# Kernel tuning notes

Hardware: AMD Instinct MI355X
Metric: run time of the kernel (lower is better)

Reference implementation:

```python
import jax, jax.numpy as jnp
import numpy as np
from jax.scipy.linalg import expm

EPS = 1e-5  # torch LayerNorm default

def _layernorm(x, g, b):
    m = x.mean(-1, keepdims=True)
    v = ((x - m) ** 2).mean(-1, keepdims=True)
    return (x - m) / jnp.sqrt(v + EPS) * g + b

def setup_inputs() -> dict:
    H, S, K = 1024, 64, 3
    B, T = 4, 4096
    key = jax.random.key(0)
    ks = jax.random.split(key, 12)
    sc = 0.02
    inp = {
        'x': jax.random.normal(ks[0], (B, T, H), jnp.float32),
        'A': -jnp.abs(jax.random.normal(ks[1], (S, S), jnp.float32) * sc),
        'dt_A': jnp.asarray(0.1, jnp.float32),
        'B_w': jax.random.normal(ks[2], (S, H), jnp.float32) * sc,
        'B_b': jnp.zeros((S,), jnp.float32),
        'C_w': jax.random.normal(ks[3], (S, H), jnp.float32) * sc,
        'C_b': jnp.zeros((S,), jnp.float32),
        'D_w': jax.random.normal(ks[4], (H, S), jnp.float32) * sc,
        'D_b': jnp.zeros((H,), jnp.float32),
        'conv_w': jax.random.normal(ks[5], (H, 1, K), jnp.float32) * sc,  # depthwise
        'conv_b': jnp.zeros((H,), jnp.float32),
        'gate_w': jax.random.normal(ks[6], (2 * H, H), jnp.float32) * sc,
        'gate_b': jnp.zeros((2 * H,), jnp.float32),
        'ln_in_g': jnp.ones((H,), jnp.float32),
        'ln_in_b': jnp.zeros((H,), jnp.float32),
        'ln_st_g': jnp.ones((S,), jnp.float32),
        'ln_st_b': jnp.zeros((S,), jnp.float32),
    }
    return inp

def reference(x, A, dt_A, B_w, B_b, C_w, C_b, D_w, D_b, conv_w, conv_b,
              gate_w, gate_b, ln_in_g, ln_in_b, ln_st_g, ln_st_b):
    Bt, T, H = x.shape
    K = conv_w.shape[-1]
    pad = K // 2
    x_norm = _layernorm(x, ln_in_g, ln_in_b)  # [B,T,H]
    # depthwise conv1d (groups = H), 'same' padding, residual add
    xc = jnp.transpose(x_norm, (0, 2, 1))  # [B,H,T]
    xc = jax.lax.conv_general_dilated(
        xc, conv_w, window_strides=(1,), padding=[(pad, pad)],
        dimension_numbers=('NCH', 'OIH', 'NCH'), feature_group_count=H)
    xc = xc + conv_b[None, :, None]
    x_norm = x_norm + jnp.transpose(xc, (0, 2, 1))
    # gating
    gate_all = x_norm @ gate_w.T + gate_b  # [B,T,2H]
    gate, input_gate = gate_all[..., :H], gate_all[..., H:]
    gate = jax.nn.sigmoid(gate)
    # input-dependent B, C
    Bm = (x_norm * jax.nn.sigmoid(input_gate)) @ B_w.T + B_b  # [B,T,S]
    Cm = x_norm @ C_w.T + C_b                                  # [B,T,S]
    A_bar = expm(dt_A * A)  # [S,S]
    # sequential recurrence over time via scan
    def step(state, bc):
        b_t, c_t = bc
        s = state @ A_bar + b_t
        s = _layernorm(s, ln_st_g, ln_st_b)
        return s, c_t * s
    state0 = jnp.zeros((Bt, A.shape[0]), x.dtype)
    _, ys = jax.lax.scan(step, state0,
                         (jnp.transpose(Bm, (1, 0, 2)), jnp.transpose(Cm, (1, 0, 2))))
    ssm = jnp.transpose(ys, (1, 0, 2))  # [B,T,S]
    ssm = ssm @ D_w.T + D_b             # [B,T,H]
    return ssm * gate
```

## Files before the change

kernel.cpp:

```cpp
#include <hip/hip_runtime.h>
#include <cstdint>

#define EPS 1e-5f
typedef float f32x4 __attribute__((ext_vector_type(4)));
typedef short bf8 __attribute__((ext_vector_type(8)));
typedef unsigned short u16;
typedef unsigned short u16x8 __attribute__((ext_vector_type(8)));
typedef unsigned int uint4v __attribute__((ext_vector_type(4)));

__device__ __forceinline__ u16 f2b(float f){
  unsigned x = __float_as_uint(f);
  unsigned r = x + 0x7FFFu + ((x>>16)&1u);
  return (u16)(r>>16);
}
__device__ __forceinline__ float b2f(u16 h){ return __uint_as_float(((unsigned)h)<<16); }
__device__ __forceinline__ unsigned pk2(float a, float b){
  unsigned ua = __float_as_uint(a) + 0x8000u;
  unsigned ub = __float_as_uint(b) + 0x8000u;
  return __builtin_amdgcn_perm(ub, ua, 0x07060302u);
}

#define GLL(gp, lp) __builtin_amdgcn_global_load_lds((__attribute__((address_space(1))) const void*)(gp), (__attribute__((address_space(3))) void*)(lp), 16, 0, 0)

__global__ __launch_bounds__(1024) void k_prep(const float* __restrict__ A, const float* __restrict__ dtp,
    const float* __restrict__ stg, const float* __restrict__ stb,
    float* __restrict__ abeta, u16* __restrict__ ft, float* __restrict__ dcm)
{
  __shared__ float M[4096], Ta[4096], Tb[4096], P[4096];
  __shared__ float cmn[64];
  int tid = threadIdx.x;
  float dt = dtp[0];
  for (int e=tid; e<4096; e+=1024){
    float v = dt * A[e];
    int i = e>>6, j = e&63;
    M[e] = v;
    P[e] = v + (i==j ? 1.0f : 0.0f);
    Ta[e] = v;
  }
  __syncthreads();
  float* src = Ta; float* dst = Tb;
  for (int k=2;k<=14;k++){
    float inv = 1.0f/(float)k;
    int i = tid>>4, j0 = (tid&15)*4;
    float a0=0,a1=0,a2=0,a3=0;
    for (int m2=0;m2<64;m2++){
      float f = src[i*64+m2];
      const float* Mr = &M[m2*64+j0];
      a0 += f*Mr[0]; a1 += f*Mr[1]; a2 += f*Mr[2]; a3 += f*Mr[3];
    }
    a0*=inv; a1*=inv; a2*=inv; a3*=inv;
    int base=i*64+j0;
    dst[base+0]=a0; dst[base+1]=a1; dst[base+2]=a2; dst[base+3]=a3;
    P[base+0]+=a0; P[base+1]+=a1; P[base+2]+=a2; P[base+3]+=a3;
    __syncthreads();
    float* tmp=src; src=dst; dst=tmp;
  }
  if (tid<64){
    float c0=0, ab=0; int p = tid;
    for (int q2=0;q2<64;q2++){ float ap = P[q2*64+p]; c0 += stg[q2]*ap; ab += stb[q2]*ap; }
    cmn[p] = c0*(1.0f/64.0f);
    abeta[p] = ab;
    dcm[p]    = stg[p]*P[p*64+p];
    dcm[64+p] = c0*(1.0f/64.0f);
  }
  __syncthreads();
  for (int e=tid; e<4096; e+=1024){
    int q2=e>>6, p=e&63;
    Ta[e] = stg[q2]*P[q2*64+p];
  }
  __syncthreads();
  for (int ii=0; ii<4; ii++){
    int e = tid*4+ii;
    int j = e&7, l = (e>>3)&63, kt=(e>>9)&1, mt=e>>10;
    int q2 = 16*(2*kt + (j>>2)) + 4*(l>>4) + (j&3);
    int p = 16*mt + (l&15);
    float v = (q2==p) ? 0.0f : Ta[q2*64+p];
    ft[e] = f2b(v);
  }
}

__global__ __launch_bounds__(256) void k_wcvt(const float* __restrict__ gw, const float* __restrict__ bw,
   const float* __restrict__ cw, const float* __restrict__ dw,
   u16* __restrict__ ogw, u16* __restrict__ obw, u16* __restrict__ ocw, u16* __restrict__ odw)
{
  int n = blockIdx.x*256 + threadIdx.x;
  if (n < 2097152) ogw[n] = f2b(gw[n]);
  else if (n < 2162688) obw[n-2097152] = f2b(bw[n-2097152]);
  else if (n < 2228224) ocw[n-2162688] = f2b(cw[n-2162688]);
  else odw[n-2228224] = f2b(dw[n-2228224]);
}

__global__ __launch_bounds__(256) void k_lnconv(const float* __restrict__ x, const float* __restrict__ gin,
  const float* __restrict__ bin, const float* __restrict__ cwt, const float* __restrict__ cb, u16* __restrict__ xn)
{
  __shared__ float red[10][8];
  int tid = threadIdx.x; int w = tid>>6; int lane = tid&63;
  int r0 = blockIdx.x*8;
  int bt = r0>>12, t0 = r0&4095;
  int c4 = tid*4;
  f32x4 g4 = *(const f32x4*)(gin + c4);
  f32x4 b4 = *(const f32x4*)(bin + c4);
  f32x4 vals[10];
  for (int lr=0; lr<10; lr++){
    int t = t0 - 1 + lr;
    f32x4 xv = {0,0,0,0};
    bool ok = (t>=0 && t<4096);
    if (ok) xv = *(const f32x4*)(x + (size_t)(bt*4096+t)*1024 + c4);
    float s = xv.x+xv.y+xv.z+xv.w;
    float q = xv.x*xv.x+xv.y*xv.y+xv.z*xv.z+xv.w*xv.w;
    for (int m2=1;m2<=32;m2<<=1){ s += __shfl_xor(s,m2,64); q += __shfl_xor(q,m2,64); }
    if (lane==0){ red[lr][w]=s; red[lr][4+w]=q; }
    __syncthreads();
    s = red[lr][0]+red[lr][1]+red[lr][2]+red[lr][3];
    q = red[lr][4]+red[lr][5]+red[lr][6]+red[lr][7];
    float mu = s*(1.f/1024.f);
    float var = q*(1.f/1024.f) - mu*mu;
    float rr = rsqrtf(var + EPS);
    f32x4 o = {0,0,0,0};
    if (ok){
      o.x=(xv.x-mu)*rr*g4.x+b4.x; o.y=(xv.y-mu)*rr*g4.y+b4.y;
      o.z=(xv.z-mu)*rr*g4.z+b4.z; o.w=(xv.w-mu)*rr*g4.w+b4.w;
    }
    vals[lr]=o;
  }
  float w0[4], w1[4], w2[4], cbv[4];
  for (int ii=0;ii<4;ii++){ int c = c4+ii; w0[ii]=cwt[c*3+0]; w1[ii]=cwt[c*3+1]; w2[ii]=cwt[c*3+2]; cbv[ii]=cb[c]; }
  for (int lr=1; lr<=8; lr++){
    int t = t0 + lr - 1;
    f32x4 o;
    o.x = vals[lr].x + w0[0]*vals[lr-1].x + w1[0]*vals[lr].x + w2[0]*vals[lr+1].x + cbv[0];
    o.y = vals[lr].y + w0[1]*vals[lr-1].y + w1[1]*vals[lr].y + w2[1]*vals[lr+1].y + cbv[1];
    o.z = vals[lr].z + w0[2]*vals[lr-1].z + w1[2]*vals[lr].z + w2[2]*vals[lr+1].z + cbv[2];
    o.w = vals[lr].w + w0[3]*vals[lr-1].w + w1[3]*vals[lr].w + w2[3]*vals[lr+1].w + cbv[3];
    size_t off = (size_t)(bt*4096+t)*1024 + c4;
    unsigned lo2 = (unsigned)f2b(o.x) | ((unsigned)f2b(o.y)<<16);
    unsigned hi2 = (unsigned)f2b(o.z) | ((unsigned)f2b(o.w)<<16);
    uint2 pk; pk.x=lo2; pk.y=hi2;
    *(uint2*)(xn + off) = pk;
  }
}

__global__ __launch_bounds__(256) void k_gate(const u16* __restrict__ xn, const u16* __restrict__ gw,
    const float* __restrict__ gb, u16* __restrict__ gate_o, u16* __restrict__ xg_o)
{
  __shared__ char smem[33792];
  u16* As = (u16*)smem;
  u16* Bs = (u16*)(smem + 8192);
  float* st = (float*)smem;
  int tid=threadIdx.x, w=tid>>6, l=tid&63;
  int flat = blockIdx.x + (int)gridDim.x*blockIdx.y;
  int logical = (flat&7)*256 + (flat>>3);
  int n0 = (logical&15)*128, m0 = (logical>>4)*128;
  int wr = w>>1, wc = w&1;
  f32x4 acc[4][4] = {};
  for (int kk=0; kk<32; kk++){
    int k0 = kk*32;
    for (int i2=0;i2<2;i2++){
      const char* ga = (const char*)xn + ((size_t)(m0+32*w+16*i2+(l>>2))*1024 + k0)*2 + (l&3)*16;
      GLL(ga, (char*)As + (32*w+16*i2)*64);
      const char* gbp = (const char*)gw + ((size_t)(n0+32*w+16*i2+(l>>2))*1024 + k0)*2 + (l&3)*16;
// ... 29 lines not shown
        v = v + gb4[j];
        ob[4*j+0] = f2b(1.0f/(1.0f+__expf(-v.x)));
        ob[4*j+1] = f2b(1.0f/(1.0f+__expf(-v.y)));
        ob[4*j+2] = f2b(1.0f/(1.0f+__expf(-v.z)));
        ob[4*j+3] = f2b(1.0f/(1.0f+__expf(-v.w)));
      }
    } else {
      const u16* xp = xn + (size_t)row*1024 + (n0-1024) + q*32;
      u16 xb[32];
      for (int j=0;j<4;j++){
        u16x8 t8 = *(const u16x8*)(xp + 8*j);
        for (int e=0;e<8;e++) xb[8*j+e] = t8[e];
      }
      for (int j=0;j<8;j++){
        f32x4 v = *(const f32x4*)(sp + 4*j);
        v = v + gb4[j];
        ob[4*j+0] = f2b(b2f(xb[4*j+0]) * (1.0f/(1.0f+__expf(-v.x))));
        ob[4*j+1] = f2b(b2f(xb[4*j+1]) * (1.0f/(1.0f+__expf(-v.y))));
        ob[4*j+2] = f2b(b2f(xb[4*j+2]) * (1.0f/(1.0f+__expf(-v.z))));
        ob[4*j+3] = f2b(b2f(xb[4*j+3]) * (1.0f/(1.0f+__expf(-v.w))));
      }
    }
    u16* op = isxg ? (xg_o + (size_t)row*1024 + (n0-1024) + q*32)
                   : (gate_o + (size_t)row*1024 + n0 + q*32);
    unsigned od[16];
    for (int i2=0;i2<16;i2++) od[i2] = (unsigned)ob[2*i2] | ((unsigned)ob[2*i2+1]<<16);
    uint4v s0 = {od[0],od[1],od[2],od[3]};
    uint4v s1 = {od[4],od[5],od[6],od[7]};
    uint4v s2 = {od[8],od[9],od[10],od[11]};
    uint4v s3 = {od[12],od[13],od[14],od[15]};
    *(uint4v*)(op+ 0) = s0;
    *(uint4v*)(op+ 8) = s1;
    *(uint4v*)(op+16) = s2;
    *(uint4v*)(op+24) = s3;
  }
}

__global__ __launch_bounds__(256) void k_bc(const u16* __restrict__ xg, const u16* __restrict__ xn,
   const u16* __restrict__ bw, const u16* __restrict__ cw,
   const float* __restrict__ bb, const float* __restrict__ cbias_, const float* __restrict__ abeta,
   float* __restrict__ c_ws, u16* __restrict__ cm)
{
  __shared__ u16 As[128*32], Bs[64*32];
  int tid=threadIdx.x, w=tid>>6, l=tid&63;
  int id = blockIdx.x; int half = id>>7; int m0 = (id&127)*128;
  const u16* Ap = half ? xn : xg;
  const u16* Bp = half ? cw : bw;
  f32x4 acc[2][4]={};
  for (int kk=0;kk<32;kk++){
    int k0=kk*32;
    for (int i2=0;i2<2;i2++){
      const char* ga=(const char*)Ap + ((size_t)(m0+32*w+16*i2+(l>>2))*1024+k0)*2+(l&3)*16;
      GLL(ga, (char*)As+(32*w+16*i2)*64);
    }
    { const char* gbp=(const char*)Bp + ((size_t)(16*w+(l>>2))*1024+k0)*2+(l&3)*16;
      GLL(gbp, (char*)Bs+(16*w)*64); }
    __syncthreads();
    bf8 af[2], bfr[4];
    for (int mt=0;mt<2;mt++) af[mt]=*(const bf8*)(As+(32*w+16*mt+(l&15))*32+8*(l>>4));
    for (int nt=0;nt<4;nt++) bfr[nt]=*(const bf8*)(Bs+(16*nt+(l&15))*32+8*(l>>4));
    for (int mt=0;mt<2;mt++) for(int nt=0;nt<4;nt++)
      acc[mt][nt]=__builtin_amdgcn_mfma_f32_16x16x32_bf16(af[mt],bfr[nt],acc[mt][nt],0,0,0);
    __syncthreads();
  }
  int g=l>>4, c=l&15;
  if (half==0){
    for (int nt=0;nt<4;nt++){ int n=16*nt+c; float bias=bb[n]; float ab=abeta[n];
      for(int mt=0;mt<2;mt++) for(int r=0;r<4;r++){
        int row=m0+32*w+16*mt+4*g+r; int bt=row>>12, t=row&4095;
        float v=acc[mt][nt][r]+bias + (t>0?ab:0.0f);
        c_ws[(size_t)t*256 + bt*64 + n] = v;
      }
    }
  } else {
    for (int nt=0;nt<4;nt++){ int n=16*nt+c; float bias=cbias_[n];
      for(int mt=0;mt<2;mt++) for(int r=0;r<4;r++){
        int row=m0+32*w+16*mt+4*g+r;
        cm[(size_t)row*64+n]=f2b(acc[mt][nt][r]+bias);
      }
    }
  }
}

__global__ __launch_bounds__(64,1) void k_scan(const float* __restrict__ c_ws, const u16* __restrict__ ft,
  const float* __restrict__ dcm, float* __restrict__ z_ws)
{
  __shared__ float ring[16*256];
  int l=threadIdx.x, g=l>>4, b=l&3;
  const bf8* ftv=(const bf8*)ft;
  bf8 Rb[4][2];
  for(int mt=0;mt<4;mt++)for(int kt=0;kt<2;kt++)
    Rb[mt][kt]=ftv[(mt*2+kt)*64+l];
  f32x4 D2r[4], Cm4[4];
  for(int mt=0;mt<4;mt++){
    D2r[mt] = *(const f32x4*)(dcm + 16*mt + 4*g);
    Cm4[mt] = *(const f32x4*)(dcm + 64 + 16*mt + 4*g);
  }
  const f32x4 zed = {0.f,0.f,0.f,0.f};
  f32x4 z0,z1,z2,z3;
  {
    const float* zp = c_ws + b*64 + 4*g;
    z0=*(const f32x4*)(zp+0); z1=*(const f32x4*)(zp+16); z2=*(const f32x4*)(zp+32); z3=*(const f32x4*)(zp+48);
  }
  for(int u2=1;u2<=11;u2++){
    const char* ga=(const char*)c_ws + (size_t)u2*1024 + l*16;
    GLL(ga, (char*)ring + u2*1024);
  }
  asm volatile("s_waitcnt vmcnt(0)" ::: "memory");
  unsigned laneoff;
  {
    __attribute__((address_space(3))) float* l3=( __attribute__((address_space(3))) float*)ring;
    laneoff=(unsigned)(uintptr_t)l3 + (unsigned)(b*256 + g*16);
  }
  unsigned voff = (unsigned)(((l&15)*64 + 4*g)*4);
  unsigned long long zb = (unsigned long long)(uintptr_t)z_ws;
  f32x4 cN0,cN1,cN2,cN3;
  bf8 zf0, zf1;

  {
    uint4v p0,p1;
    p0.x=pk2(z0.x,z0.y); p0.y=pk2(z0.z,z0.w); p0.z=pk2(z1.x,z1.y); p0.w=pk2(z1.z,z1.w);
    p1.x=pk2(z2.x,z2.y); p1.y=pk2(z2.z,z2.w); p1.z=pk2(z3.x,z3.y); p1.w=pk2(z3.z,z3.w);
    { union { uint4v u; bf8 h; } cv; cv.u=p0; zf0=cv.h; cv.u=p1; zf1=cv.h; }
  }

  unsigned slotr = 1024u;
  unsigned ldst  = 12u*1024u;
  const char* gsrc = (const char*)c_ws + (size_t)12*1024;

  for (int t=0; t<4096; ++t){
    asm volatile("s_waitcnt vmcnt(48)" ::: "memory");
    { unsigned ro = laneoff + slotr;
      asm volatile("ds_read_b128 %0, %4 offset:0\n\t"
                   "ds_read_b128 %1, %4 offset:64\n\t"
                   "ds_read_b128 %2, %4 offset:128\n\t"
                   "ds_read_b128 %3, %4 offset:192"
                   : "=v"(cN0),"=v"(cN1),"=v"(cN2),"=v"(cN3) : "v"(ro) : "memory"); }
    GLL(gsrc + (size_t)l*16, (char*)ring + ldst);
    f32x4 u0=__builtin_amdgcn_mfma_f32_16x16x32_bf16(Rb[0][0],zf0,zed,0,0,0);
    f32x4 u1=__builtin_amdgcn_mfma_f32_16x16x32_bf16(Rb[1][0],zf0,zed,0,0,0);
    f32x4 u2=__builtin_amdgcn_mfma_f32_16x16x32_bf16(Rb[2][0],zf0,zed,0,0,0);
    f32x4 u3=__builtin_amdgcn_mfma_f32_16x16x32_bf16(Rb[3][0],zf0,zed,0,0,0);
    u0=__builtin_amdgcn_mfma_f32_16x16x32_bf16(Rb[0][1],zf1,u0,0,0,0);
    u1=__builtin_amdgcn_mfma_f32_16x16x32_bf16(Rb[1][1],zf1,u1,0,0,0);
    u2=__builtin_amdgcn_mfma_f32_16x16x32_bf16(Rb[2][1],zf1,u2,0,0,0);
    u3=__builtin_amdgcn_mfma_f32_16x16x32_bf16(Rb[3][1],zf1,u3,0,0,0);
    float s, rr;
    {
      f32x4 s4=(z0+z1)+(z2+z3);
      s=(s4.x+s4.y)+(s4.z+s4.w);
      f32x4 qa=z0*z0; qa=z1*z1+qa;
      f32x4 qb=z2*z2; qb=z3*z3+qb;
      f32x4 q4=qa+qb;
      float q=(q4.x+q4.y)+(q4.z+q4.w);
      float sB=s, qB=q;
      asm("v_permlane16_swap_b32 %0, %1" : "+v"(s), "+v"(sB));
      asm("v_permlane16_swap_b32 %0, %1" : "+v"(q), "+v"(qB));
      s+=sB; q+=qB;
      float sC=s, qC=q;
      asm("v_permlane32_swap_b32 %0, %1" : "+v"(s), "+v"(sC));
      asm("v_permlane32_swap_b32 %0, %1" : "+v"(q), "+v"(qC));
      s+=sC; q+=qC;
      float mu=s*(1.f/64.f);
      float var=q*(1.f/64.f)-mu*mu;
      rr=rsqrtf(var+EPS);
    }
    asm volatile("s_waitcnt lgkmcnt(0)" : "+v"(cN0),"+v"(cN1),"+v"(cN2),"+v"(cN3) :: "memory");
    f32x4 h0 = (z0*D2r[0] - Cm4[0]*s)*rr + cN0;
    f32x4 h1 = (z1*D2r[1] - Cm4[1]*s)*rr + cN1;
    f32x4 h2 = (z2*D2r[2] - Cm4[2]*s)*rr + cN2;
    f32x4 h3 = (z3*D2r[3] - Cm4[3]*s)*rr + cN3;
    asm volatile("global_store_dwordx4 %0, %1, %5\n\t"
                 "global_store_dwordx4 %0, %2, %5 offset:64\n\t"
                 "global_store_dwordx4 %0, %3, %5 offset:128\n\t"
                 "global_store_dwordx4 %0, %4, %5 offset:192"
                 :: "v"(voff), "v"(z0), "v"(z1), "v"(z2), "v"(z3), "s"(zb) : "memory");
    voff += 4096u;
    slotr = (slotr + 1024u) & 16383u;
    ldst  = (ldst  + 1024u) & 16383u;
    gsrc += 1024;
    z0 = u0*rr + h0;
    z1 = u1*rr + h1;
    z2 = u2*rr + h2;
    z3 = u3*rr + h3;
    uint4v p0,p1;
    p0.x=pk2(z0.x,z0.y); p0.y=pk2(z0.z,z0.w); p0.z=pk2(z1.x,z1.y); p0.w=pk2(z1.z,z1.w);
    p1.x=pk2(z2.x,z2.y); p1.y=pk2(z2.z,z2.w); p1.z=pk2(z3.x,z3.y); p1.w=pk2(z3.z,z3.w);
    { union { uint4v u; bf8 h; } cv; cv.u=p0; zf0=cv.h; cv.u=p1; zf1=cv.h; }
  }
}

__global__ __launch_bounds__(256) void k_y(const float* __restrict__ z_ws, const u16* __restrict__ cm,
  const float* __restrict__ stg, const float* __restrict__ stb, u16* __restrict__ y)
{
  int tid=threadIdx.x, w=tid>>6, l=tid&63;
  int token = blockIdx.x*4 + w;
  int bt = token>>12, t = token&4095;
  float zv = z_ws[(size_t)t*1024 + bt*64 + l];
  float s=zv, q=zv*zv;
  for (int m2=1;m2<=32;m2<<=1){ s += __shfl_xor(s,m2,64); q += __shfl_xor(q,m2,64); }
  float mu=s*(1.f/64.f), var=q*(1.f/64.f)-mu*mu, rr=rsqrtf(var+EPS);
  float sv=(zv-mu)*rr*stg[l]+stb[l];
  y[(size_t)token*64 + l] = f2b(sv * b2f(cm[(size_t)token*64+l]));
}

__global__ __launch_bounds__(256) void k_out(const u16* __restrict__ y, const u16* __restrict__ dw,
   const float* __restrict__ db, const u16* __restrict__ gate, float* __restrict__ out)
{
  __shared__ float tr[4][16][68];
  int tid=threadIdx.x, w=tid>>6, l=tid&63, g=l>>4, c=l&15;
  int n0=blockIdx.x*64, m0=blockIdx.y*64;
  int mrow = m0 + 16*w + c;
  bf8 af0=*(const bf8*)(y + (size_t)mrow*64 + 8*g);
  bf8 af1=*(const bf8*)(y + (size_t)mrow*64 + 32 + 8*g);
  f32x4 acc[4];
  for(int nt=0;nt<4;nt++){
    int n=n0+16*nt+c;
    bf8 b0=*(const bf8*)(dw + (size_t)n*64 + 8*g);
    bf8 b1=*(const bf8*)(dw + (size_t)n*64 + 32 + 8*g);
    f32x4 a={0,0,0,0};
    a=__builtin_amdgcn_mfma_f32_16x16x32_bf16(af0,b0,a,0,0,0);
    a=__builtin_amdgcn_mfma_f32_16x16x32_bf16(af1,b1,a,0,0,0);
    acc[nt]=a+db[n];
  }
  for(int nt=0;nt<4;nt++) for(int r=0;r<4;r++) tr[w][4*g+r][16*nt+c]=acc[nt][r];
  __syncthreads();
  int lr=l>>2, cc0=(l&3)*16;
  int grow=m0+16*w+lr;
  const u16* gp = gate + (size_t)grow*1024 + n0 + cc0;
  u16x8 g0=*(const u16x8*)(gp), g1=*(const u16x8*)(gp+8);
  float* op = out + (size_t)grow*1024 + n0 + cc0;
  float vv[16];
  for(int j2=0;j2<16;j2++){
    u16 gb16 = (j2<8)? g0[j2] : g1[j2-8];
    vv[j2]=tr[w][lr][cc0+j2]*b2f(gb16);
  }
  for(int j2=0;j2<4;j2++){
    f32x4 ov={vv[4*j2],vv[4*j2+1],vv[4*j2+2],vv[4*j2+3]};
    *(f32x4*)(op+4*j2)=ov;
  }
}

extern "C" void kernel_launch(void* const* d_in, const int* in_sizes, int n_in,
                              void* d_out, int out_size, void* d_ws, size_t ws_size,
                              hipStream_t stream) {
  const float* x=(const float*)d_in[0];
  const float* A=(const float*)d_in[1];
  const float* dt=(const float*)d_in[2];
  const float* B_w=(const float*)d_in[3];
  const float* B_b=(const float*)d_in[4];
  const float* C_w=(const float*)d_in[5];
  const float* C_b=(const float*)d_in[6];
  const float* D_w=(const float*)d_in[7];
  const float* D_b=(const float*)d_in[8];
  const float* conv_w=(const float*)d_in[9];
  const float* conv_b=(const float*)d_in[10];
  const float* gate_w=(const float*)d_in[11];
  const float* gate_b=(const float*)d_in[12];
  const float* ln_in_g=(const float*)d_in[13];
  const float* ln_in_b=(const float*)d_in[14];
  const float* ln_st_g=(const float*)d_in[15];
  const float* ln_st_b=(const float*)d_in[16];
  char* ws=(char*)d_ws;
  u16* xn   =(u16*)(ws);
  u16* xg   =(u16*)(ws+33554432);
  u16* gate =(u16*)(ws+67108864);
  u16* gwb  =(u16*)(ws+100663296);
  u16* bwb  =(u16*)(ws+104857600);
  u16* cwb  =(u16*)(ws+104988672);
  u16* dwb  =(u16*)(ws+105119744);
  u16* cm   =(u16*)(ws+105250816);
  float* c_ws=(float*)(ws+107347968);
  float* z_ws=(float*)(ws+111558656);
  u16* y    =(u16*)(ws+128335872);
  float* abeta=(float*)(ws+130433024);
  u16* ft   =(u16*)(ws+130433280);
  float* dcm =(float*)(ws+130433280+8192);
  float* out=(float*)d_out;

  hipLaunchKernelGGL(k_prep,  dim3(1),      dim3(1024),0,stream, A, dt, ln_st_g, ln_st_b, abeta, ft, dcm);
  hipLaunchKernelGGL(k_wcvt,  dim3(8960),   dim3(256), 0,stream, gate_w,B_w,C_w,D_w, gwb,bwb,cwb,dwb);
  hipLaunchKernelGGL(k_lnconv,dim3(2048),   dim3(256), 0,stream, x, ln_in_g, ln_in_b, conv_w, conv_b, xn);
  hipLaunchKernelGGL(k_gate,  dim3(16,128), dim3(256), 0,stream, xn,gwb,gate_b,gate,xg);
  hipLaunchKernelGGL(k_bc,    dim3(256),    dim3(256), 0,stream, xg,xn,bwb,cwb,B_b,C_b,abeta,c_ws,cm);
  hipLaunchKernelGGL(k_scan,  dim3(1),      dim3(64),  0,stream, c_ws, ft, dcm, z_ws);
  hipLaunchKernelGGL(k_y,     dim3(4096),   dim3(256), 0,stream, z_ws,cm,ln_st_g,ln_st_b,y);
  hipLaunchKernelGGL(k_out,   dim3(16,256), dim3(256), 0,stream, y,dwb,D_b,gate,out);
}
```

Measured before the change: 1.732 ms.

## Replace LDS ring prefetch in scan with register-rotated direct global loads

The sequential scan kernel drops its LDS ring buffer, which was filled with global_load_lds and read back with ds_read every step. It now keeps four register sets of prefetched per-step inputs and issues direct global loads three or four steps ahead, gated by a vmcnt wait in a loop unrolled by four. This removes the LDS round trip and lgkmcnt wait from the serial critical path. It also limits the z stores to the 4 of 16 lane groups that write meaningful rows, cutting redundant store traffic. The catch is a much shallower prefetch distance, and vmcnt now counts those stores too, so global load latency may be exposed more often.

```diff
diff --git a/kernel.cpp b/kernel.cpp
--- a/kernel.cpp
+++ b/kernel.cpp
@@ -274,7 +274,6 @@
 __global__ __launch_bounds__(64,1) void k_scan(const float* __restrict__ c_ws, const u16* __restrict__ ft,
   const float* __restrict__ dcm, float* __restrict__ z_ws)
 {
-  __shared__ float ring[16*256];
   int l=threadIdx.x, g=l>>4, b=l&3;
   const bf8* ftv=(const bf8*)ft;
   bf8 Rb[4][2];
@@ -291,19 +290,10 @@
     const float* zp = c_ws + b*64 + 4*g;
     z0=*(const f32x4*)(zp+0); z1=*(const f32x4*)(zp+16); z2=*(const f32x4*)(zp+32); z3=*(const f32x4*)(zp+48);
   }
-  for(int u2=1;u2<=11;u2++){
-    const char* ga=(const char*)c_ws + (size_t)u2*1024 + l*16;
-    GLL(ga, (char*)ring + u2*1024);
-  }
-  asm volatile("s_waitcnt vmcnt(0)" ::: "memory");
-  unsigned laneoff;
-  {
-    __attribute__((address_space(3))) float* l3=( __attribute__((address_space(3))) float*)ring;
-    laneoff=(unsigned)(uintptr_t)l3 + (unsigned)(b*256 + g*16);
-  }
   unsigned voff = (unsigned)(((l&15)*64 + 4*g)*4);
   unsigned long long zb = (unsigned long long)(uintptr_t)z_ws;
-  f32x4 cN0,cN1,cN2,cN3;
+  unsigned long long cbse = (unsigned long long)(uintptr_t)c_ws;
+  bool stl = ((l&15) < 4);
   bf8 zf0, zf1;
 
   {
@@ -313,70 +303,91 @@
     { union { uint4v u; bf8 h; } cv; cv.u=p0; zf0=cv.h; cv.u=p1; zf1=cv.h; }
   }
 
-  unsigned slotr = 1024u;
-  unsigned ldst  = 12u*1024u;
-  const char* gsrc = (const char*)c_ws + (size_t)12*1024;
-
-  for (int t=0; t<4096; ++t){
-    asm volatile("s_waitcnt vmcnt(48)" ::: "memory");
-    { unsigned ro = laneoff + slotr;
-      asm volatile("ds_read_b128 %0, %4 offset:0\n\t"
-                   "ds_read_b128 %1, %4 offset:64\n\t"
-                   "ds_read_b128 %2, %4 offset:128\n\t"
-                   "ds_read_b128 %3, %4 offset:192"
-                   : "=v"(cN0),"=v"(cN1),"=v"(cN2),"=v"(cN3) : "v"(ro) : "memory"); }
-    GLL(gsrc + (size_t)l*16, (char*)ring + ldst);
-    f32x4 u0=__builtin_amdgcn_mfma_f32_16x16x32_bf16(Rb[0][0],zf0,zed,0,0,0);
-    f32x4 u1=__builtin_amdgcn_mfma_f32_16x16x32_bf16(Rb[1][0],zf0,zed,0,0,0);
-    f32x4 u2=__builtin_amdgcn_mfma_f32_16x16x32_bf16(Rb[2][0],zf0,zed,0,0,0);
-    f32x4 u3=__builtin_amdgcn_mfma_f32_16x16x32_bf16(Rb[3][0],zf0,zed,0,0,0);
-    u0=__builtin_amdgcn_mfma_f32_16x16x32_bf16(Rb[0][1],zf1,u0,0,0,0);
-    u1=__builtin_amdgcn_mfma_f32_16x16x32_bf16(Rb[1][1],zf1,u1,0,0,0);
-    u2=__builtin_amdgcn_mfma_f32_16x16x32_bf16(Rb[2][1],zf1,u2,0,0,0);
-    u3=__builtin_amdgcn_mfma_f32_16x16x32_bf16(Rb[3][1],zf1,u3,0,0,0);
-    float s, rr;
-    {
-      f32x4 s4=(z0+z1)+(z2+z3);
-      s=(s4.x+s4.y)+(s4.z+s4.w);
-      f32x4 qa=z0*z0; qa=z1*z1+qa;
-      f32x4 qb=z2*z2; qb=z3*z3+qb;
-      f32x4 q4=qa+qb;
-      float q=(q4.x+q4.y)+(q4.z+q4.w);
-      float sB=s, qB=q;
-      asm("v_permlane16_swap_b32 %0, %1" : "+v"(s), "+v"(sB));
-      asm("v_permlane16_swap_b32 %0, %1" : "+v"(q), "+v"(qB));
-      s+=sB; q+=qB;
-      float sC=s, qC=q;
-      asm("v_permlane32_swap_b32 %0, %1" : "+v"(s), "+v"(sC));
-      asm("v_permlane32_swap_b32 %0, %1" : "+v"(q), "+v"(qC));
-      s+=sC; q+=qC;
-      float mu=s*(1.f/64.f);
-      float var=q*(1.f/64.f)-mu*mu;
-      rr=rsqrtf(var+EPS);
-    }
-    asm volatile("s_waitcnt lgkmcnt(0)" : "+v"(cN0),"+v"(cN1),"+v"(cN2),"+v"(cN3) :: "memory");
-    f32x4 h0 = (z0*D2r[0] - Cm4[0]*s)*rr + cN0;
-    f32x4 h1 = (z1*D2r[1] - Cm4[1]*s)*rr + cN1;
-    f32x4 h2 = (z2*D2r[2] - Cm4[2]*s)*rr + cN2;
-    f32x4 h3 = (z3*D2r[3] - Cm4[3]*s)*rr + cN3;
-    asm volatile("global_store_dwordx4 %0, %1, %5\n\t"
-                 "global_store_dwordx4 %0, %2, %5 offset:64\n\t"
-                 "global_store_dwordx4 %0, %3, %5 offset:128\n\t"
-                 "global_store_dwordx4 %0, %4, %5 offset:192"
-                 :: "v"(voff), "v"(z0), "v"(z1), "v"(z2), "v"(z3), "s"(zb) : "memory");
-    voff += 4096u;
-    slotr = (slotr + 1024u) & 16383u;
-    ldst  = (ldst  + 1024u) & 16383u;
-    gsrc += 1024;
-    z0 = u0*rr + h0;
-    z1 = u1*rr + h1;
-    z2 = u2*rr + h2;
-    z3 = u3*rr + h3;
-    uint4v p0,p1;
-    p0.x=pk2(z0.x,z0.y); p0.y=pk2(z0.z,z0.w); p0.z=pk2(z1.x,z1.y); p0.w=pk2(z1.z,z1.w);
-    p1.x=pk2(z2.x,z2.y); p1.y=pk2(z2.z,z2.w); p1.z=pk2(z3.x,z3.y); p1.w=pk2(z3.z,z3.w);
-    { union { uint4v u; bf8 h; } cv; cv.u=p0; zf0=cv.h; cv.u=p1; zf1=cv.h; }
-  }
+  unsigned cvo = (unsigned)((b*64 + 4*g)*4);
+  unsigned voA = 1024u*1 + cvo, voB = 1024u*2 + cvo, voC = 1024u*3 + cvo, voD = 1024u*4 + cvo;
+  f32x4 cA0,cA1,cA2,cA3, cB0,cB1,cB2,cB3, cC0,cC1,cC2,cC3, cD0,cD1,cD2,cD3;
+#define CLOAD(R0,R1,R2,R3, VO) \
+  asm volatile("global_load_dwordx4 %0, %4, %5 offset:0\n\t" \
+               "global_load_dwordx4 %1, %4, %5 offset:64\n\t" \
+               "global_load_dwordx4 %2, %4, %5 offset:128\n\t" \
+               "global_load_dwordx4 %3, %4, %5 offset:192" \
+               : "=&v"(R0),"=&v"(R1),"=&v"(R2),"=&v"(R3) \
+               : "v"(VO), "s"(cbse) : "memory")
+  CLOAD(cA0,cA1,cA2,cA3, voA);  voA += 4096u;
+  CLOAD(cB0,cB1,cB2,cB3, voB);  voB += 4096u;
+  CLOAD(cC0,cC1,cC2,cC3, voC);  voC += 4096u;
+  CLOAD(cD0,cD1,cD2,cD3, voD);  voD += 4096u;
+  asm volatile("s_waitcnt vmcnt(0)" ::: "memory");
+
+#define STEP(T, C0,C1,C2,C3, VO) do { \
+  asm volatile("s_waitcnt vmcnt(24)" : "+v"(C0),"+v"(C1),"+v"(C2),"+v"(C3) :: "memory"); \
+   \
+  f32x4 u0=__builtin_amdgcn_mfma_f32_16x16x32_bf16(Rb[0][0],zf0,zed,0,0,0); \
+  f32x4 u1=__builtin_amdgcn_mfma_f32_16x16x32_bf16(Rb[1][0],zf0,zed,0,0,0); \
+  f32x4 u2=__builtin_amdgcn_mfma_f32_16x16x32_bf16(Rb[2][0],zf0,zed,0,0,0); \
+  f32x4 u3=__builtin_amdgcn_mfma_f32_16x16x32_bf16(Rb[3][0],zf0,zed,0,0,0); \
+  u0=__builtin_amdgcn_mfma_f32_16x16x32_bf16(Rb[0][1],zf1,u0,0,0,0); \
+  u1=__builtin_amdgcn_mfma_f32_16x16x32_bf16(Rb[1][1],zf1,u1,0,0,0); \
+  u2=__builtin_amdgcn_mfma_f32_16x16x32_bf16(Rb[2][1],zf1,u2,0,0,0); \
+  u3=__builtin_amdgcn_mfma_f32_16x16x32_bf16(Rb[3][1],zf1,u3,0,0,0); \
+   \
+  float s, rr; \
+  { \
+    f32x4 s4=(z0+z1)+(z2+z3); \
+    s=(s4.x+s4.y)+(s4.z+s4.w); \
+    f32x4 qa=z0*z0; qa=z1*z1+qa; \
+    f32x4 qb=z2*z2; qb=z3*z3+qb; \
+    f32x4 q4=qa+qb; \
+    float q=(q4.x+q4.y)+(q4.z+q4.w); \
+    float sB=s, qB=q; \
+    asm("v_permlane16_swap_b32 %0, %1" : "+v"(s), "+v"(sB)); \
+    asm("v_permlane16_swap_b32 %0, %1" : "+v"(q), "+v"(qB)); \
+    s+=sB; q+=qB; \
+    float sC=s, qC=q; \
+    asm("v_permlane32_swap_b32 %0, %1" : "+v"(s), "+v"(sC)); \
+    asm("v_permlane32_swap_b32 %0, %1" : "+v"(q), "+v"(qC)); \
+    s+=sC; q+=qC; \
+    float mu=s*(1.f/64.f); \
+    float var=q*(1.f/64.f)-mu*mu; \
+    rr=rsqrtf(var+EPS); \
+  } \
+   \
+  f32x4 h0 = (z0*D2r[0] - Cm4[0]*s)*rr + C0; \
+  f32x4 h1 = (z1*D2r[1] - Cm4[1]*s)*rr + C1; \
+  f32x4 h2 = (z2*D2r[2] - Cm4[2]*s)*rr + C2; \
+  f32x4 h3 = (z3*D2r[3] - Cm4[3]*s)*rr + C3; \
+   \
+  if (stl){ \
+    asm volatile("global_store_dwordx4 %0, %1, %5\n\t" \
+                 "global_store_dwordx4 %0, %2, %5 offset:64\n\t" \
+                 "global_store_dwordx4 %0, %3, %5 offset:128\n\t" \
+                 "global_store_dwordx4 %0, %4, %5 offset:192" \
+                 :: "v"(voff), "v"(z0), "v"(z1), "v"(z2), "v"(z3), "s"(zb) : "memory"); \
+  } \
+  voff += 4096u; \
+   \
+  CLOAD(C0,C1,C2,C3, VO); \
+  VO += 4096u; \
+   \
+  z0 = u0*rr + h0; \
+  z1 = u1*rr + h1; \
+  z2 = u2*rr + h2; \
+  z3 = u3*rr + h3; \
+   \
+  uint4v p0,p1; \
+  p0.x=pk2(z0.x,z0.y); p0.y=pk2(z0.z,z0.w); p0.z=pk2(z1.x,z1.y); p0.w=pk2(z1.z,z1.w); \
+  p1.x=pk2(z2.x,z2.y); p1.y=pk2(z2.z,z2.w); p1.z=pk2(z3.x,z3.y); p1.w=pk2(z3.z,z3.w); \
+  { union { uint4v u; bf8 h; } cv; cv.u=p0; zf0=cv.h; cv.u=p1; zf1=cv.h; } \
+} while(0)
+
+  for (int t=0; t<4096; t+=4){
+    STEP(t,   cA0,cA1,cA2,cA3, voA);
+    STEP(t+1, cB0,cB1,cB2,cB3, voB);
+    STEP(t+2, cC0,cC1,cC2,cC3, voC);
+    STEP(t+3, cD0,cD1,cD2,cD3, voD);
+  }
+#undef STEP
+#undef CLOAD
 }
 
 __global__ __launch_bounds__(256) void k_y(const float* __restrict__ z_ws, const u16* __restrict__ cm,
```

Measured after the change: 1.912 ms. 1.1x slower.

## Two-step the sequential scan using precomputed squared transition and input projections

Applied to the files above, without the earlier changes.

The single-wave recurrence is reformulated to advance two timesteps per dependent chain. It precomputes the centred transition matrix and its square in k_prep, and the projections of the per-step inputs through both matrices in a new parallel kernel k_fc. The scan then issues both MFMA products from the same state and shortens the serial latency per pair of steps. State is now stored as bf16 in a new layout that k_y reads. This adds an extra kernel, more global traffic and more bf16 rounding of the projected terms, which risks accuracy drift over 4096 steps.

```diff
diff --git a/kernel.cpp b/kernel.cpp
--- a/kernel.cpp
+++ b/kernel.cpp
@@ -24,7 +24,8 @@
 
 __global__ __launch_bounds__(1024) void k_prep(const float* __restrict__ A, const float* __restrict__ dtp,
     const float* __restrict__ stg, const float* __restrict__ stb,
-    float* __restrict__ abeta, u16* __restrict__ ft, float* __restrict__ dcm)
+    float* __restrict__ abeta, u16* __restrict__ ft, float* __restrict__ dcm,
+    float* __restrict__ m1g, float* __restrict__ m2g)
 {
   __shared__ float M[4096], Ta[4096], Tb[4096], P[4096];
   __shared__ float cmn[64];
@@ -60,22 +61,37 @@
     for (int q2=0;q2<64;q2++){ float ap = P[q2*64+p]; c0 += stg[q2]*ap; ab += stb[q2]*ap; }
     cmn[p] = c0*(1.0f/64.0f);
     abeta[p] = ab;
-    dcm[p]    = stg[p]*P[p*64+p];
-    dcm[64+p] = c0*(1.0f/64.0f);
   }
   __syncthreads();
   for (int e=tid; e<4096; e+=1024){
     int q2=e>>6, p=e&63;
-    Ta[e] = stg[q2]*P[q2*64+p];
+    Ta[e] = stg[q2]*P[e] - cmn[p];
   }
   __syncthreads();
+  {
+    int i = tid>>4, j0 = (tid&15)*4;
+    float a0=0,a1=0,a2=0,a3=0;
+    for (int m2=0;m2<64;m2++){
+      float f = Ta[i*64+m2];
+      const float* Mr = &Ta[m2*64+j0];
+      a0 += f*Mr[0]; a1 += f*Mr[1]; a2 += f*Mr[2]; a3 += f*Mr[3];
+    }
+    int base=i*64+j0;
+    Tb[base+0]=a0; Tb[base+1]=a1; Tb[base+2]=a2; Tb[base+3]=a3;
+  }
+  __syncthreads();
+  for (int e=tid; e<4096; e+=1024){ m1g[e]=Ta[e]; m2g[e]=Tb[e]; }
+  if (tid<64){
+    dcm[tid]    = Ta[tid*64+tid];
+    dcm[64+tid] = Tb[tid*64+tid];
+  }
   for (int ii=0; ii<4; ii++){
     int e = tid*4+ii;
     int j = e&7, l = (e>>3)&63, kt=(e>>9)&1, mt=e>>10;
     int q2 = 16*(2*kt + (j>>2)) + 4*(l>>4) + (j&3);
     int p = 16*mt + (l&15);
-    float v = (q2==p) ? 0.0f : Ta[q2*64+p];
-    ft[e] = f2b(v);
+    ft[e]      = f2b(q2==p ? 0.0f : Ta[q2*64+p]);
+    ft[e+4096] = f2b(q2==p ? 0.0f : Tb[q2*64+p]);
   }
 }
 
@@ -271,121 +287,182 @@
   }
 }
 
+__global__ __launch_bounds__(256) void k_fc(const float* __restrict__ c_ws,
+  const float* __restrict__ m1g, const float* __restrict__ m2g,
+  u16* __restrict__ fc, u16* __restrict__ ffc)
+{
+  __shared__ float M1s[4096], M2s[4096], Cs[4096];
+  int tid=threadIdx.x; int t0=blockIdx.x*16;
+  for (int e=tid; e<4096; e+=256){
+    M1s[e]=m1g[e]; M2s[e]=m2g[e];
+    int row=e>>6, q=e&63;
+    Cs[e]=c_ws[(size_t)(t0+(row>>2))*256 + (row&3)*64 + q];
+  }
+  __syncthreads();
+  int row=tid>>2, pq=tid&3;
+  const float* cr=&Cs[row*64];
+  float f1[16], f2[16];
+  #pragma unroll
+  for (int k2=0;k2<16;k2++){ f1[k2]=0.f; f2[k2]=0.f; }
+  for (int q=0;q<64;q++){
+    float cq=cr[q];
+    const float* r1=&M1s[q*64+pq*16];
+    const float* r2=&M2s[q*64+pq*16];
+    #pragma unroll
+    for (int k2=0;k2<16;k2++){ f1[k2]+=cq*r1[k2]; f2[k2]+=cq*r2[k2]; }
+  }
+  int t=t0+(row>>2), b=row&3;
+  #pragma unroll
+  for (int gp=0;gp<4;gp++){
+    uint2 o1, o2;
+    o1.x = pk2(f1[gp*4+0], f1[gp*4+1]); o1.y = pk2(f1[gp*4+2], f1[gp*4+3]);
+    o2.x = pk2(f2[gp*4+0], f2[gp*4+1]); o2.y = pk2(f2[gp*4+2], f2[gp*4+3]);
+    size_t off = (size_t)t*256 + (size_t)((b*4+gp)*16 + pq*4);
+    *(uint2*)(fc+off) = o1;
+    *(uint2*)(ffc+off) = o2;
+  }
+}
+
 __global__ __launch_bounds__(64,1) void k_scan(const float* __restrict__ c_ws, const u16* __restrict__ ft,
-  const float* __restrict__ dcm, float* __restrict__ z_ws)
-{
-  __shared__ float ring[16*256];
+  const float* __restrict__ dcm, const u16* __restrict__ fc_ws, const u16* __restrict__ ffc_ws,
+  u16* __restrict__ zb16)
+{
   int l=threadIdx.x, g=l>>4, b=l&3;
   const bf8* ftv=(const bf8*)ft;
-  bf8 Rb[4][2];
-  for(int mt=0;mt<4;mt++)for(int kt=0;kt<2;kt++)
-    Rb[mt][kt]=ftv[(mt*2+kt)*64+l];
-  f32x4 D2r[4], Cm4[4];
+  bf8 O1f[4][2], O2f[4][2];
+  for(int mt=0;mt<4;mt++)for(int kt=0;kt<2;kt++){
+    O1f[mt][kt]=ftv[(mt*2+kt)*64+l];
+    O2f[mt][kt]=ftv[(8+mt*2+kt)*64+l];
+  }
+  f32x4 D1r[4], D2r[4];
   for(int mt=0;mt<4;mt++){
-    D2r[mt] = *(const f32x4*)(dcm + 16*mt + 4*g);
-    Cm4[mt] = *(const f32x4*)(dcm + 64 + 16*mt + 4*g);
-  }
-  const f32x4 zed = {0.f,0.f,0.f,0.f};
-  f32x4 z0,z1,z2,z3;
-  {
-    const float* zp = c_ws + b*64 + 4*g;
-    z0=*(const f32x4*)(zp+0); z1=*(const f32x4*)(zp+16); z2=*(const f32x4*)(zp+32); z3=*(const f32x4*)(zp+48);
-  }
-  for(int u2=1;u2<=11;u2++){
-    const char* ga=(const char*)c_ws + (size_t)u2*1024 + l*16;
-    GLL(ga, (char*)ring + u2*1024);
-  }
+    D1r[mt]=*(const f32x4*)(dcm+16*mt+4*g);
+    D2r[mt]=*(const f32x4*)(dcm+64+16*mt+4*g);
+  }
+  const f32x4 zed={0.f,0.f,0.f,0.f};
+  unsigned cbase=(unsigned)((b*64+4*g)*4);
+  unsigned fbase=(unsigned)((b*4+g)*32);
+  unsigned long long cbse=(unsigned long long)(uintptr_t)c_ws;
+  unsigned long long fbse=(unsigned long long)(uintptr_t)fc_ws;
+  unsigned long long hbse=(unsigned long long)(uintptr_t)ffc_ws;
+  unsigned long long zb  =(unsigned long long)(uintptr_t)zb16;
+  bool stl = ((l&15)<4);
+
+#define MF(Aop,Bop,Cin) __builtin_amdgcn_mfma_f32_16x16x32_bf16(Aop,Bop,Cin,0,0,0)
+#define UNPK(D, U, i0, i1) { D.x=__uint_as_float((U)[i0]<<16); D.y=__uint_as_float((U)[i0]&0xffff0000u); \
+                             D.z=__uint_as_float((U)[i1]<<16); D.w=__uint_as_float((U)[i1]&0xffff0000u); }
+#define PACKZ(Z0,Z1,Z2,Z3, P0,P1) { \
+  P0.x=pk2(Z0.x,Z0.y); P0.y=pk2(Z0.z,Z0.w); P0.z=pk2(Z1.x,Z1.y); P0.w=pk2(Z1.z,Z1.w); \
+  P1.x=pk2(Z2.x,Z2.y); P1.y=pk2(Z2.z,Z2.w); P1.z=pk2(Z3.x,Z3.y); P1.w=pk2(Z3.z,Z3.w); }
+#define REDUCE_RR(Z0,Z1,Z2,Z3, RR) { \
+  f32x4 s4=((Z0)+(Z1))+((Z2)+(Z3)); float s=(s4.x+s4.y)+(s4.z+s4.w); \
+  f32x4 qa=(Z0)*(Z0); qa=(Z1)*(Z1)+qa; f32x4 qb=(Z2)*(Z2); qb=(Z3)*(Z3)+qb; f32x4 q4=qa+qb; \
+  float q=(q4.x+q4.y)+(q4.z+q4.w); \
+  float sB=s,qB=q; asm("v_permlane16_swap_b32 %0, %1":"+v"(s),"+v"(sB)); \
+  asm("v_permlane16_swap_b32 %0, %1":"+v"(q),"+v"(qB)); s+=sB;q+=qB; \
+  float sC=s,qC=q; asm("v_permlane32_swap_b32 %0, %1":"+v"(s),"+v"(sC)); \
+  asm("v_permlane32_swap_b32 %0, %1":"+v"(q),"+v"(qC)); s+=sC;q+=qC; \
+  float mu=s*(1.f/64.f); float var=q*(1.f/64.f)-mu*mu; RR=rsqrtf(var+EPS); }
+#define LD_C(R0,R1,R2,R3, OFF) asm volatile( \
+  "global_load_dwordx4 %0, %4, %5 offset:0\n\t" \
+  "global_load_dwordx4 %1, %4, %5 offset:64\n\t" \
+  "global_load_dwordx4 %2, %4, %5 offset:128\n\t" \
+  "global_load_dwordx4 %3, %4, %5 offset:192" \
+  : "=&v"(R0),"=&v"(R1),"=&v"(R2),"=&v"(R3) : "v"(OFF), "s"(cbse) : "memory")
+#define LD_C2(R0,R1,R2,R3, OFF) asm volatile( \
+  "global_load_dwordx4 %0, %4, %5 offset:1024\n\t" \
+  "global_load_dwordx4 %1, %4, %5 offset:1088\n\t" \
+  "global_load_dwordx4 %2, %4, %5 offset:1152\n\t" \
+  "global_load_dwordx4 %3, %4, %5 offset:1216" \
+  : "=&v"(R0),"=&v"(R1),"=&v"(R2),"=&v"(R3) : "v"(OFF), "s"(cbse) : "memory")
+#define LD_F(Ra,Rb, OFF, BASE) asm volatile( \
+  "global_load_dwordx4 %0, %2, %3 offset:0\n\t" \
+  "global_load_dwordx4 %1, %2, %3 offset:16" \
+  : "=&v"(Ra),"=&v"(Rb) : "v"(OFF), "s"(BASE) : "memory")
+#define LD_F2(Ra,Rb, OFF, BASE) asm volatile( \
+  "global_load_dwordx4 %0, %2, %3 offset:512\n\t" \
+  "global_load_dwordx4 %1, %2, %3 offset:528" \
+  : "=&v"(Ra),"=&v"(Rb) : "v"(OFF), "s"(BASE) : "memory")
+#define ST_Z(P0,P1, VO) if(stl){ asm volatile( \
+  "global_store_dwordx4 %0, %1, %3\n\t" \
+  "global_store_dwordx4 %0, %2, %3 offset:16" \
+  :: "v"(VO), "v"(P0), "v"(P1), "s"(zb) : "memory"); }
+
+  f32x4 z00,z01,z02,z03;
+  { const float* zp = c_ws + b*64 + 4*g;
+    z00=*(const f32x4*)(zp); z01=*(const f32x4*)(zp+16); z02=*(const f32x4*)(zp+32); z03=*(const f32x4*)(zp+48); }
+  f32x4 Gs0,Gs1,Gs2,Gs3;
+  { const uint4v* fp=(const uint4v*)((const char*)fc_ws + fbase);
+    uint4v ga=fp[0], gb2=fp[1];
+    UNPK(Gs0, ga,0,1); UNPK(Gs1, ga,2,3); UNPK(Gs2, gb2,0,1); UNPK(Gs3, gb2,2,3); }
+  float rr; REDUCE_RR(z00,z01,z02,z03, rr);
+  bf8 zf0, zf1;
+  { uint4v p0,p1; PACKZ(Gs0,Gs1,Gs2,Gs3,p0,p1);
+    union{uint4v u; bf8 h;}cv; cv.u=p0; zf0=cv.h; cv.u=p1; zf1=cv.h; }
+  unsigned voff = fbase;
+  { uint4v q0,q1; PACKZ(z00,z01,z02,z03,q0,q1); ST_Z(q0,q1, voff); }
+  voff += 512u;
+  f32x4 cA10,cA11,cA12,cA13, cA20,cA21,cA22,cA23;
+  f32x4 cB10,cB11,cB12,cB13, cB20,cB21,cB22,cB23;
+  uint4v fA1a,fA1b, fA2a,fA2b, hA1a,hA1b;
+  uint4v fB1a,fB1b, fB2a,fB2b, hB1a,hB1b;
+  unsigned cOfA = 1024u + cbase,  fOfA = 512u + fbase;
+  unsigned cOfB = 3072u + cbase,  fOfB = 1536u + fbase;
+  LD_C (cA10,cA11,cA12,cA13, cOfA); LD_C2(cA20,cA21,cA22,cA23, cOfA);
+  LD_F (fA1a,fA1b, fOfA, fbse); LD_F2(fA2a,fA2b, fOfA, fbse); LD_F(hA1a,hA1b, fOfA, hbse);
+  cOfA += 4096u; fOfA += 2048u;
+  LD_C (cB10,cB11,cB12,cB13, cOfB); LD_C2(cB20,cB21,cB22,cB23, cOfB);
+  LD_F (fB1a,fB1b, fOfB, fbse); LD_F2(fB2a,fB2b, fOfB, fbse); LD_F(hB1a,hB1b, fOfB, hbse);
+  cOfB += 4096u; fOfB += 2048u;
   asm volatile("s_waitcnt vmcnt(0)" ::: "memory");
-  unsigned laneoff;
-  {
-    __attribute__((address_space(3))) float* l3=( __attribute__((address_space(3))) float*)ring;
-    laneoff=(unsigned)(uintptr_t)l3 + (unsigned)(b*256 + g*16);
-  }
-  unsigned voff = (unsigned)(((l&15)*64 + 4*g)*4);
-  unsigned long long zb = (unsigned long long)(uintptr_t)z_ws;
-  f32x4 cN0,cN1,cN2,cN3;
-  bf8 zf0, zf1;
-
-  {
-    uint4v p0,p1;
-    p0.x=pk2(z0.x,z0.y); p0.y=pk2(z0.z,z0.w); p0.z=pk2(z1.x,z1.y); p0.w=pk2(z1.z,z1.w);
-    p1.x=pk2(z2.x,z2.y); p1.y=pk2(z2.z,z2.w); p1.z=pk2(z3.x,z3.y); p1.w=pk2(z3.z,z3.w);
-    { union { uint4v u; bf8 h; } cv; cv.u=p0; zf0=cv.h; cv.u=p1; zf1=cv.h; }
-  }
-
-  unsigned slotr = 1024u;
-  unsigned ldst  = 12u*1024u;
-  const char* gsrc = (const char*)c_ws + (size_t)12*1024;
-
-  for (int t=0; t<4096; ++t){
-    asm volatile("s_waitcnt vmcnt(48)" ::: "memory");
-    { unsigned ro = laneoff + slotr;
-      asm volatile("ds_read_b128 %0, %4 offset:0\n\t"
-                   "ds_read_b128 %1, %4 offset:64\n\t"
-                   "ds_read_b128 %2, %4 offset:128\n\t"
-                   "ds_read_b128 %3, %4 offset:192"
-                   : "=v"(cN0),"=v"(cN1),"=v"(cN2),"=v"(cN3) : "v"(ro) : "memory"); }
-    GLL(gsrc + (size_t)l*16, (char*)ring + ldst);
-    f32x4 u0=__builtin_amdgcn_mfma_f32_16x16x32_bf16(Rb[0][0],zf0,zed,0,0,0);
-    f32x4 u1=__builtin_amdgcn_mfma_f32_16x16x32_bf16(Rb[1][0],zf0,zed,0,0,0);
-    f32x4 u2=__builtin_amdgcn_mfma_f32_16x16x32_bf16(Rb[2][0],zf0,zed,0,0,0);
-    f32x4 u3=__builtin_amdgcn_mfma_f32_16x16x32_bf16(Rb[3][0],zf0,zed,0,0,0);
-    u0=__builtin_amdgcn_mfma_f32_16x16x32_bf16(Rb[0][1],zf1,u0,0,0,0);
-    u1=__builtin_amdgcn_mfma_f32_16x16x32_bf16(Rb[1][1],zf1,u1,0,0,0);
-    u2=__builtin_amdgcn_mfma_f32_16x16x32_bf16(Rb[2][1],zf1,u2,0,0,0);
-    u3=__builtin_amdgcn_mfma_f32_16x16x32_bf16(Rb[3][1],zf1,u3,0,0,0);
-    float s, rr;
-    {
-      f32x4 s4=(z0+z1)+(z2+z3);
-      s=(s4.x+s4.y)+(s4.z+s4.w);
-      f32x4 qa=z0*z0; qa=z1*z1+qa;
-      f32x4 qb=z2*z2; qb=z3*z3+qb;
-      f32x4 q4=qa+qb;
-      float q=(q4.x+q4.y)+(q4.z+q4.w);
-      float sB=s, qB=q;
-      asm("v_permlane16_swap_b32 %0, %1" : "+v"(s), "+v"(sB));
-      asm("v_permlane16_swap_b32 %0, %1" : "+v"(q), "+v"(qB));
-      s+=sB; q+=qB;
-      float sC=s, qC=q;
-      asm("v_permlane32_swap_b32 %0, %1" : "+v"(s), "+v"(sC));
-      asm("v_permlane32_swap_b32 %0, %1" : "+v"(q), "+v"(qC));
-      s+=sC; q+=qC;
-      float mu=s*(1.f/64.f);
-      float var=q*(1.f/64.f)-mu*mu;
-      rr=rsqrtf(var+EPS);
-    }
-    asm volatile("s_waitcnt lgkmcnt(0)" : "+v"(cN0),"+v"(cN1),"+v"(cN2),"+v"(cN3) :: "memory");
-    f32x4 h0 = (z0*D2r[0] - Cm4[0]*s)*rr + cN0;
-    f32x4 h1 = (z1*D2r[1] - Cm4[1]*s)*rr + cN1;
-    f32x4 h2 = (z2*D2r[2] - Cm4[2]*s)*rr + cN2;
-    f32x4 h3 = (z3*D2r[3] - Cm4[3]*s)*rr + cN3;
-    asm volatile("global_store_dwordx4 %0, %1, %5\n\t"
-                 "global_store_dwordx4 %0, %2, %5 offset:64\n\t"
-                 "global_store_dwordx4 %0, %3, %5 offset:128\n\t"
-                 "global_store_dwordx4 %0, %4, %5 offset:192"
-                 :: "v"(voff), "v"(z0), "v"(z1), "v"(z2), "v"(z3), "s"(zb) : "memory");
-    voff += 4096u;
-    slotr = (slotr + 1024u) & 16383u;
-    ldst  = (ldst  + 1024u) & 16383u;
-    gsrc += 1024;
-    z0 = u0*rr + h0;
-    z1 = u1*rr + h1;
-    z2 = u2*rr + h2;
-    z3 = u3*rr + h3;
-    uint4v p0,p1;
-    p0.x=pk2(z0.x,z0.y); p0.y=pk2(z0.z,z0.w); p0.z=pk2(z1.x,z1.y); p0.w=pk2(z1.z,z1.w);
-    p1.x=pk2(z2.x,z2.y); p1.y=pk2(z2.z,z2.w); p1.z=pk2(z3.x,z3.y); p1.w=pk2(z3.z,z3.w);
-    { union { uint4v u; bf8 h; } cv; cv.u=p0; zf0=cv.h; cv.u=p1; zf1=cv.h; }
-  }
-}
-
-__global__ __launch_bounds__(256) void k_y(const float* __restrict__ z_ws, const u16* __restrict__ cm,
+
+#define ITER(C10,C11,C12,C13,C20,C21,C22,C23, F1a,F1b,F2a,F2b, H1a,H1b, COF, FOF) do{ \
+  asm volatile("s_waitcnt vmcnt(18)" : "+v"(C10),"+v"(C11),"+v"(C12),"+v"(C13), \
+     "+v"(C20),"+v"(C21),"+v"(C22),"+v"(C23), "+v"(F1a),"+v"(F1b),"+v"(F2a),"+v"(F2b), \
+     "+v"(H1a),"+v"(H1b) :: "memory"); \
+  f32x4 Ho0=MF(O1f[0][0],zf0,zed), Ho1=MF(O1f[1][0],zf0,zed), Ho2=MF(O1f[2][0],zf0,zed), Ho3=MF(O1f[3][0],zf0,zed); \
+  f32x4 Ko0=MF(O2f[0][0],zf0,zed), Ko1=MF(O2f[1][0],zf0,zed), Ko2=MF(O2f[2][0],zf0,zed), Ko3=MF(O2f[3][0],zf0,zed); \
+  Ho0=MF(O1f[0][1],zf1,Ho0); Ho1=MF(O1f[1][1],zf1,Ho1); Ho2=MF(O1f[2][1],zf1,Ho2); Ho3=MF(O1f[3][1],zf1,Ho3); \
+  Ko0=MF(O2f[0][1],zf1,Ko0); Ko1=MF(O2f[1][1],zf1,Ko1); Ko2=MF(O2f[2][1],zf1,Ko2); Ko3=MF(O2f[3][1],zf1,Ko3); \
+  f32x4 zA0=Gs0*rr+C10, zA1=Gs1*rr+C11, zA2=Gs2*rr+C12, zA3=Gs3*rr+C13; \
+  float rr1; REDUCE_RR(zA0,zA1,zA2,zA3, rr1); \
+  f32x4 Pa0,Pa1,Pa2,Pa3; UNPK(Pa0,F1a,0,1); UNPK(Pa1,F1a,2,3); UNPK(Pa2,F1b,0,1); UNPK(Pa3,F1b,2,3); \
+  f32x4 Pb0,Pb1,Pb2,Pb3; UNPK(Pb0,F2a,0,1); UNPK(Pb1,F2a,2,3); UNPK(Pb2,F2b,0,1); UNPK(Pb3,F2b,2,3); \
+  f32x4 Q0,Q1,Q2,Q3;     UNPK(Q0,H1a,0,1);  UNPK(Q1,H1a,2,3);  UNPK(Q2,H1b,0,1);  UNPK(Q3,H1b,2,3); \
+  f32x4 T0=Q0*rr1+Pb0, T1=Q1*rr1+Pb1, T2=Q2*rr1+Pb2, T3=Q3*rr1+Pb3; \
+  f32x4 H0=Gs0*D1r[0]+Ho0, H1=Gs1*D1r[1]+Ho1, H2=Gs2*D1r[2]+Ho2, H3=Gs3*D1r[3]+Ho3; \
+  f32x4 Gm0=H0*rr+Pa0, Gm1=H1*rr+Pa1, Gm2=H2*rr+Pa2, Gm3=H3*rr+Pa3; \
+  f32x4 zB0=Gm0*rr1+C20, zB1=Gm1*rr1+C21, zB2=Gm2*rr1+C22, zB3=Gm3*rr1+C23; \
+  float rr2; REDUCE_RR(zB0,zB1,zB2,zB3, rr2); \
+  f32x4 K0=Gs0*D2r[0]+Ko0, K1=Gs1*D2r[1]+Ko1, K2=Gs2*D2r[2]+Ko2, K3=Gs3*D2r[3]+Ko3; \
+  float rrp=rr*rr1; \
+  Gs0=K0*rrp+T0; Gs1=K1*rrp+T1; Gs2=K2*rrp+T2; Gs3=K3*rrp+T3; \
+  { uint4v q0,q1; PACKZ(zA0,zA1,zA2,zA3,q0,q1); ST_Z(q0,q1, voff); } \
+  { uint4v q0,q1; PACKZ(zB0,zB1,zB2,zB3,q0,q1); ST_Z(q0,q1, voff+512u); } \
+  voff += 1024u; \
+  LD_C (C10,C11,C12,C13, COF); LD_C2(C20,C21,C22,C23, COF); \
+  LD_F (F1a,F1b, FOF, fbse); LD_F2(F2a,F2b, FOF, fbse); LD_F(H1a,H1b, FOF, hbse); \
+  COF += 4096u; FOF += 2048u; \
+  { uint4v p0,p1; PACKZ(Gs0,Gs1,Gs2,Gs3,p0,p1); \
+    union{uint4v u; bf8 h;}cv; cv.u=p0; zf0=cv.h; cv.u=p1; zf1=cv.h; } \
+  rr = rr2; \
+}while(0)
+
+  for (int i=0; i<2048; i+=2){
+    ITER(cA10,cA11,cA12,cA13,cA20,cA21,cA22,cA23, fA1a,fA1b,fA2a,fA2b, hA1a,hA1b, cOfA, fOfA);
+    ITER(cB10,cB11,cB12,cB13,cB20,cB21,cB22,cB23, fB1a,fB1b,fB2a,fB2b, hB1a,hB1b, cOfB, fOfB);
+  }
+#undef ITER
+}
+
+__global__ __launch_bounds__(256) void k_y(const u16* __restrict__ zb16, const u16* __restrict__ cm,
   const float* __restrict__ stg, const float* __restrict__ stb, u16* __restrict__ y)
 {
   int tid=threadIdx.x, w=tid>>6, l=tid&63;
   int token = blockIdx.x*4 + w;
   int bt = token>>12, t = token&4095;
-  float zv = z_ws[(size_t)t*1024 + bt*64 + l];
+  int gg=(l>>2)&3, mt=l>>4, rrq=l&3;
+  float zv = b2f(zb16[(size_t)t*256 + (size_t)((bt*4+gg)*16 + mt*4 + rrq)]);
   float s=zv, q=zv*zv;
   for (int m2=1;m2<=32;m2<<=1){ s += __shfl_xor(s,m2,64); q += __shfl_xor(q,m2,64); }
   float mu=s*(1.f/64.f), var=q*(1.f/64.f)-mu*mu, rr=rsqrtf(var+EPS);
@@ -460,19 +537,24 @@
   u16* dwb  =(u16*)(ws+105119744);
   u16* cm   =(u16*)(ws+105250816);
   float* c_ws=(float*)(ws+107347968);
-  float* z_ws=(float*)(ws+111558656);
+  u16* zb16  =(u16*)(ws+111558656);
+  u16* fc_ws =(u16*)(ws+111558656+4194304);
+  u16* ffc_ws=(u16*)(ws+111558656+6295552);
+  float* m1g =(float*)(ws+111558656+8396800);
+  float* m2g =(float*)(ws+111558656+8413184);
+  float* dcm =(float*)(ws+111558656+8429568);
   u16* y    =(u16*)(ws+128335872);
   float* abeta=(float*)(ws+130433024);
   u16* ft   =(u16*)(ws+130433280);
-  float* dcm =(float*)(ws+130433280+8192);
   float* out=(float*)d_out;
 
-  hipLaunchKernelGGL(k_prep,  dim3(1),      dim3(1024),0,stream, A, dt, ln_st_g, ln_st_b, abeta, ft, dcm);
+  hipLaunchKernelGGL(k_prep,  dim3(1),      dim3(1024),0,stream, A, dt, ln_st_g, ln_st_b, abeta, ft, dcm, m1g, m2g);
   hipLaunchKernelGGL(k_wcvt,  dim3(8960),   dim3(256), 0,stream, gate_w,B_w,C_w,D_w, gwb,bwb,cwb,dwb);
   hipLaunchKernelGGL(k_lnconv,dim3(2048),   dim3(256), 0,stream, x, ln_in_g, ln_in_b, conv_w, conv_b, xn);
   hipLaunchKernelGGL(k_gate,  dim3(16,128), dim3(256), 0,stream, xn,gwb,gate_b,gate,xg);
   hipLaunchKernelGGL(k_bc,    dim3(256),    dim3(256), 0,stream, xg,xn,bwb,cwb,B_b,C_b,abeta,c_ws,cm);
-  hipLaunchKernelGGL(k_scan,  dim3(1),      dim3(64),  0,stream, c_ws, ft, dcm, z_ws);
-  hipLaunchKernelGGL(k_y,     dim3(4096),   dim3(256), 0,stream, z_ws,cm,ln_st_g,ln_st_b,y);
+  hipLaunchKernelGGL(k_fc,    dim3(256),    dim3(256), 0,stream, c_ws, m1g, m2g, fc_ws, ffc_ws);
+  hipLaunchKernelGGL(k_scan,  dim3(1),      dim3(64),  0,stream, c_ws, ft, dcm, fc_ws, ffc_ws, zb16);
+  hipLaunchKernelGGL(k_y,     dim3(4096),   dim3(256), 0,stream, zb16,cm,ln_st_g,ln_st_b,y);
   hipLaunchKernelGGL(k_out,   dim3(16,256), dim3(256), 0,stream, y,dwb,D_b,gate,out);
 }
```

Result: slower. 2.290 ms (+32.2%).
